# Kernel optimization log

Hardware: AMD Instinct MI355X
Metric: run time of the kernel (lower is better)

The kernel has to match this reference:

```python
import jax, jax.numpy as jnp
import numpy as np
from math import sqrt

B = 32          # batch
C = 81          # label_num (class 0 = background, skipped)
N = 15130       # number of default boxes
K = 200         # max_num candidates per class
MAX_OUT = 200   # max_output boxes per image
SCORE_THR = 0.05
CRITERIA = 0.45
SCALE_XY = 0.1
SCALE_WH = 0.2
NEG_INF = -1e30


def make_dboxes_xywh():
    """Replicates DefaultBoxes for figsize (1200,1200), SSD-R34 COCO config."""
    fig = 1200
    feat = [50, 25, 13, 7, 3, 3]
    scales = [int(s * fig / 300) for s in [21, 45, 99, 153, 207, 261, 315]]
    aspect_ratios = [[2], [2, 3], [2, 3], [2, 3], [2], [2]]
    boxes = []
    for idx, f in enumerate(feat):
        step = int(fig / f)
        fk = fig // step  # == f for this config
        sk1 = scales[idx] / fig
        sk2 = scales[idx + 1] / fig
        sk3 = sqrt(sk1 * sk2)
        sizes = [(sk1, sk1), (sk3, sk3)]
        for a in aspect_ratios[idx]:
            w, h = sk1 * sqrt(a), sk1 / sqrt(a)
            sizes.append((w, h))
            sizes.append((h, w))
        for (w, h) in sizes:
            for i in range(f):
                for j in range(f):
                    cx, cy = (j + 0.5) / fk, (i + 0.5) / fk
                    boxes.append((cx, cy, w, h))
    d = np.clip(np.array(boxes, dtype=np.float32), 0.0, 1.0)
    assert d.shape[0] == N
    return d[None, :, :]  # [1, N, 4]


def setup_inputs() -> dict:
    key = jax.random.key(0)
    k1, k2 = jax.random.split(key)
    bboxes_in = jax.random.normal(k1, (B, 4, N), dtype=jnp.float32)
    scores_in = jax.random.normal(k2, (B, C, N), dtype=jnp.float32)
    dboxes_xywh = jnp.asarray(make_dboxes_xywh())
    return {"bboxes_in": bboxes_in, "scores_in": scores_in, "dboxes_xywh": dboxes_xywh}


def scale_back_batch(bboxes_in, scores_in, dboxes_xywh):
    b = jnp.transpose(bboxes_in, (0, 2, 1))            # [B, N, 4]
    xy = SCALE_XY * b[..., :2] * dboxes_xywh[..., 2:] + dboxes_xywh[..., :2]
    wh = jnp.exp(SCALE_WH * b[..., 2:]) * dboxes_xywh[..., 2:]
    ltrb = jnp.concatenate([xy - 0.5 * wh, xy + 0.5 * wh], axis=-1)  # [B, N, 4]
    probs = jax.nn.softmax(jnp.transpose(scores_in, (0, 2, 1)), axis=-1)  # [B, N, C]
    return ltrb, probs


def pairwise_iou(b):
    """Faithful to calc_iou_tensor: the masked_fill_ on delta.clone() is a no-op
    in the original, so negative deltas are NOT clamped."""
    lt = jnp.maximum(b[:, None, :2], b[None, :, :2])
    rb = jnp.minimum(b[:, None, 2:], b[None, :, 2:])
    d = rb - lt
    inter = d[..., 0] * d[..., 1]
    area = (b[:, 2] - b[:, 0]) * (b[:, 3] - b[:, 1])
    return inter / (area[:, None] + area[None, :] - inter)  # [K, K]


def nms_one_class(boxes, score):
    """boxes [N,4], score [N] -> kept boxes [K,4], kept scores [K] (NEG_INF = dropped).
    Greedy NMS over the top-K scores in descending order, matching the original
    while-loop (ascending sort + pop-from-end)."""
    s = jnp.where(score > SCORE_THR, score, NEG_INF)
    top_s, top_i = jax.lax.top_k(s, K)         # descending
    bk = boxes[top_i]                          # [K, 4]
    iou = pairwise_iou(bk)                     # [K, K]
    rng = jnp.arange(K)
    keep0 = top_s > NEG_INF

    def body(i, keep):
        suppress = keep[i] & (iou[i] >= CRITERIA) & (rng > i)
        return keep & ~suppress

    keep = jax.lax.fori_loop(0, K, body, keep0)
    return bk, jnp.where(keep, top_s, NEG_INF)


def decode_image(boxes, probs):
    """boxes [N,4], probs [N,C] -> (boxes [MAX_OUT,4], labels [MAX_OUT], scores [MAX_OUT])."""
    cls_scores = jnp.transpose(probs[:, 1:])                    # [C-1, N] (skip background)
    bks, ss = jax.vmap(nms_one_class, in_axes=(None, 0))(boxes, cls_scores)  # [C-1,K,4],[C-1,K]
    labels = jnp.repeat(jnp.arange(1, C, dtype=jnp.int32), K)   # [(C-1)*K]
    flat_s = ss.reshape(-1)
    top_s, top_i = jax.lax.top_k(flat_s, MAX_OUT)               # global top max_output
    out_boxes = bks.reshape(-1, 4)[top_i]
    out_labels = labels[top_i]
    valid = top_s > NEG_INF
    return (jnp.where(valid[:, None], out_boxes, 0.0),
            jnp.where(valid, out_labels, 0),
            jnp.where(valid, top_s, 0.0))


def reference(bboxes_in, scores_in, dboxes_xywh):
    ltrb, probs = scale_back_batch(bboxes_in, scores_in, dboxes_xywh)
    boxes, labels, scores = jax.vmap(decode_image)(ltrb, probs)
    return boxes, labels, scores  # [B,MAX_OUT,4], [B,MAX_OUT] int32, [B,MAX_OUT]
```

## Files before the change

### kernel.cpp

```cpp
#include <hip/hip_runtime.h>
#include <cstdint>
#include <cstddef>

#define BATCH 32
#define NCLS 81
#define NFG 80
#define NBOX 15130
#define NCHUNK 60
#define TOPK 200
#define NTASK (BATCH * NFG)
#define NEG_INF -1e30f
#define GCAP 1024
#define SORTCAP 1024
#define LCAP 1920
#define SCORE_THR 0.05f
#define CRITERIA 0.45f

__global__ __launch_bounds__(256) void k1_fused(
    const float* __restrict__ bboxes,
    const float* __restrict__ scores,
    const float* __restrict__ dboxes,
    float4* __restrict__ ltrb,
    unsigned long long* __restrict__ gcand,
    int* __restrict__ gcnt)
{
    const int blk = blockIdx.x;
    const int b = blk / NCHUNK;
    const int chunk = blk - b * NCHUNK;
    const int tid = threadIdx.x;
    const int n = chunk * 256 + tid;

    __shared__ unsigned long long list[LCAP];
    __shared__ int lcnt;
    __shared__ int ccnt[NFG];
    __shared__ int cbase[NFG];

    if (tid == 0) lcnt = 0;
    if (tid < NFG) ccnt[tid] = 0;
    __syncthreads();

    float m = 0.f, s = 1.f, thrv = 1e30f;
    const float* sc = scores;

    if (n < NBOX) {
        const float* bb = bboxes + (size_t)b * 4 * NBOX + n;
        float bx = bb[0];
        float by = bb[NBOX];
        float bw = bb[2 * (size_t)NBOX];
        float bh = bb[3 * (size_t)NBOX];
        float4 d = reinterpret_cast<const float4*>(dboxes)[n];
        float xx = __fadd_rn(__fmul_rn(__fmul_rn(0.1f, bx), d.z), d.x);
        float yy = __fadd_rn(__fmul_rn(__fmul_rn(0.1f, by), d.w), d.y);
        float wx = __fmul_rn(expf(__fmul_rn(0.2f, bw)), d.z);
        float wy = __fmul_rn(expf(__fmul_rn(0.2f, bh)), d.w);
        float4 o;
        o.x = __fsub_rn(xx, __fmul_rn(0.5f, wx));
        o.y = __fsub_rn(yy, __fmul_rn(0.5f, wy));
        o.z = __fadd_rn(xx, __fmul_rn(0.5f, wx));
        o.w = __fadd_rn(yy, __fmul_rn(0.5f, wy));
        ltrb[(size_t)b * NBOX + n] = o;

        sc = scores + (size_t)b * NCLS * NBOX + n;
        {
            float vals[NCLS];
#pragma unroll
            for (int c = 0; c < NCLS; ++c) vals[c] = sc[(size_t)c * NBOX];
            m = vals[0];
#pragma unroll
            for (int c = 1; c < NCLS; ++c) m = fmaxf(m, vals[c]);
            float ss = 0.0f;
#pragma unroll
            for (int c = 0; c < NCLS; ++c) ss = __fadd_rn(ss, expf(__fsub_rn(vals[c], m)));
            s = ss;
        }
        thrv = __fsub_rn(__fadd_rn(m, logf(__fmul_rn(0.05f, s))), 1e-3f);
    }

    if (n < NBOX) {
        uintptr_t scu = (uintptr_t)sc;
        asm volatile("" : "+v"(scu));
        const float* scv = (const float*)scu;
        for (int c0 = 1; c0 < NCLS; c0 += 16) {
            float vt[16];
#pragma unroll
            for (int u = 0; u < 16; ++u) {
                int c = c0 + u;
                vt[u] = (c < NCLS) ? scv[(size_t)c * NBOX] : -1e30f;
            }
#pragma unroll
            for (int u = 0; u < 16; ++u) {
                int c = c0 + u;
                if (vt[u] > thrv) {
                    float p = __fdiv_rn(expf(__fsub_rn(vt[u], m)), s);
                    if (p > SCORE_THR) {
                        int e = atomicAdd(&lcnt, 1);
                        if (e < LCAP) {
                            list[e] = ((unsigned long long)__float_as_uint(p) << 32) |
                                      ((unsigned long long)(unsigned)(c - 1) << 24) |
                                      (unsigned long long)(unsigned)n;
                        } else {
                            int pos = atomicAdd(&gcnt[b * NFG + (c - 1)], 1);
                            if (pos < GCAP)
                                gcand[(size_t)(b * NFG + (c - 1)) * GCAP + pos] =
                                    ((unsigned long long)__float_as_uint(p) << 32) |
                                    (unsigned long long)(0xFFFFFFFFu - (unsigned)n);
                        }
                    }
                }
            }
        }
    }
    __syncthreads();

    const int E = min(lcnt, LCAP);

    for (int i = tid; i < E; i += 256) {
        int c = (int)((list[i] >> 24) & 0xFF);
        atomicAdd(&ccnt[c], 1);
    }
    __syncthreads();

    if (tid < NFG && ccnt[tid] > 0)
        cbase[tid] = atomicAdd(&gcnt[b * NFG + tid], ccnt[tid]);
    __syncthreads();
    if (tid < NFG) ccnt[tid] = 0;
    __syncthreads();

    for (int i = tid; i < E; i += 256) {
        unsigned long long e = list[i];
        int c = (int)((e >> 24) & 0xFF);
        unsigned nn = (unsigned)(e & 0xFFFFFF);
        int pos = cbase[c] + atomicAdd(&ccnt[c], 1);
        if (pos < GCAP) {
            unsigned pb = (unsigned)(e >> 32);
            gcand[(size_t)(b * NFG + c) * GCAP + pos] =
                ((unsigned long long)pb << 32) |
                (unsigned long long)(0xFFFFFFFFu - nn);
        }
    }
}

template<int NR, int J, int K>
__device__ __forceinline__ void bstep(unsigned long long (&it)[NR], const int lane) {
    if constexpr (J >= 64) {
        constexpr int M = J >> 6;
#pragma unroll
        for (int r = 0; r < NR; ++r) {
            const int rp = r ^ M;
            if (rp > r) {
                const bool desc = (((unsigned)(r << 6) & (unsigned)K) == 0u);
                unsigned long long a = it[r], bb = it[rp];
                if (desc ? (a < bb) : (a > bb)) { it[r] = bb; it[rp] = a; }
            }
        }
    } else {
#pragma unroll
        for (int r = 0; r < NR; ++r) {
            unsigned long long a = it[r];
            unsigned long long bb = __shfl_xor(a, J, 64);
            const unsigned i = ((unsigned)(r << 6)) | (unsigned)lane;
            const bool desc = ((i & (unsigned)K) == 0u);
            const bool lower = ((lane & J) == 0);
            it[r] = ((desc == lower) ? (a >= bb) : (a <= bb)) ? a : bb;
        }
    }
}

template<int NR, int K, int J>
__device__ __forceinline__ void bstage(unsigned long long (&it)[NR], const int lane) {
    bstep<NR, J, K>(it, lane);
    if constexpr (J > 1) bstage<NR, K, (J >> 1)>(it, lane);
}

template<int NR>
__device__ __forceinline__ void bsort(unsigned long long (&it)[NR], const int lane,
                                      const unsigned kmax) {
    bstage<NR, 2, 1>(it, lane);
    if (kmax >= 4)   bstage<NR, 4, 2>(it, lane);
    if (kmax >= 8)   bstage<NR, 8, 4>(it, lane);
    if (kmax >= 16)  bstage<NR, 16, 8>(it, lane);
    if (kmax >= 32)  bstage<NR, 32, 16>(it, lane);
    if (kmax >= 64)  bstage<NR, 64, 32>(it, lane);
    if constexpr (NR >= 4) {
        if (kmax >= 128) bstage<NR, 128, 64>(it, lane);
        if (kmax >= 256) bstage<NR, 256, 128>(it, lane);
    }
    if constexpr (NR >= 8)  { if (kmax >= 512)  bstage<NR, 512, 256>(it, lane); }
    if constexpr (NR >= 16) { if (kmax >= 1024) bstage<NR, 1024, 512>(it, lane); }
}

__global__ __launch_bounds__(64) void k2_nms(
    const unsigned long long* __restrict__ gcand,
    const int* __restrict__ gcnt,
    const float4* __restrict__ ltrb,
    float* __restrict__ cls_scores,
    int* __restrict__ cls_idx)
{
    const int t = blockIdx.x;
    const int b = t / NFG;
    const int lane = threadIdx.x;

    const int cl = min(gcnt[t], SORTCAP);
    const unsigned long long* gc = gcand + (size_t)t * GCAP;

    unsigned kmax = 2;
    while (kmax < (unsigned)cl) kmax <<= 1;

    unsigned long long top4[4];
    if (cl <= 256) {
        unsigned long long it[4];
#pragma unroll
        for (int r = 0; r < 4; ++r) {
            const int i = (r << 6) + lane;
            it[r] = (i < cl) ? gc[i] : 0ULL;
        }
        bsort<4>(it, lane, kmax);
#pragma unroll
        for (int r = 0; r < 4; ++r) top4[r] = it[r];
    } else if (cl <= 512) {
        unsigned long long it[8];
#pragma unroll
        for (int r = 0; r < 8; ++r) {
            const int i = (r << 6) + lane;
            it[r] = (i < cl) ? gc[i] : 0ULL;
        }
        bsort<8>(it, lane, kmax);
#pragma unroll
        for (int r = 0; r < 4; ++r) top4[r] = it[r];
    } else {
        unsigned long long it[16];
#pragma unroll
        for (int r = 0; r < 16; ++r) {
            const int i = (r << 6) + lane;
            it[r] = (i < cl) ? gc[i] : 0ULL;
        }
        bsort<16>(it, lane, kmax);
#pragma unroll
        for (int r = 0; r < 4; ++r) top4[r] = it[r];
    }

    const int mk = min(cl, TOPK);

    float4 myb[4];
    float mya[4], myp[4];
    int myn[4];
#pragma unroll
    for (int r = 0; r < 4; ++r) {
        const int i = (r << 6) + lane;
        myb[r] = make_float4(0.f, 0.f, 0.f, 0.f);
        mya[r] = 0.f; myp[r] = 0.f; myn[r] = 0;
        if (i < mk) {
            const unsigned long long key = top4[r];
            const unsigned n = 0xFFFFFFFFu - (unsigned)(key & 0xFFFFFFFFull);
            const float4 bx = ltrb[(size_t)b * NBOX + n];
            myb[r] = bx;
            mya[r] = __fmul_rn(__fsub_rn(bx.z, bx.x), __fsub_rn(bx.w, bx.y));
            myp[r] = __uint_as_float((unsigned)(key >> 32));
            myn[r] = b * NBOX + (int)n;
        }
    }

    auto maskBits = [](int r) -> unsigned long long {
        if (r <= 0) return 0ULL;
        if (r >= 64) return ~0ULL;
        return (1ULL << r) - 1ULL;
    };
    unsigned long long kw0 = maskBits(mk);
    unsigned long long kw1 = maskBits(mk - 64);
    unsigned long long kw2 = maskBits(mk - 128);
    unsigned long long kw3 = maskBits(mk - 192);

#define RDLANE_F(V, SL) __uint_as_float((unsigned)__builtin_amdgcn_readlane((int)__float_as_uint(V), (SL)))

#define NMS_QUAD(KWQ, Q)                                                           \
    {                                                                              \
        const int i0 = (Q) << 6;                                                   \
        const int i1 = min(mk, i0 + 64);                                           \
        for (int i = i0; i < i1; ++i) {                                            \
            if ((KWQ >> (i - i0)) & 1ULL) {                                        \
                const int sl = i - i0;                                             \
                const float bix = RDLANE_F(myb[Q].x, sl);                          \
                const float biy = RDLANE_F(myb[Q].y, sl);                          \
                const float biz = RDLANE_F(myb[Q].z, sl);                          \
                const float biw = RDLANE_F(myb[Q].w, sl);                          \
                const float ai  = RDLANE_F(mya[Q], sl);                            \
                _Pragma("unroll")                                                  \
                for (int q2 = 0; q2 < 4; ++q2) {                                   \
                    const int j = (q2 << 6) + lane;                                \
                    const float4 bj = myb[q2];                                     \
                    const float ltx = fmaxf(bix, bj.x), lty = fmaxf(biy, bj.y);    \
                    const float rbx = fminf(biz, bj.z), rby = fminf(biw, bj.w);    \
                    const float dx = __fsub_rn(rbx, ltx), dy = __fsub_rn(rby, lty);\
                    const float inter = __fmul_rn(dx, dy);                         \
                    const float uni = __fsub_rn(__fadd_rn(ai, mya[q2]), inter);    \
                    const float iou = __fdiv_rn(inter, uni);                       \
                    const unsigned long long sup =                                 \
                        __ballot((iou >= CRITERIA) && (j > i));                    \
                    if (q2 == 0) kw0 &= ~sup;                                      \
                    else if (q2 == 1) kw1 &= ~sup;                                 \
                    else if (q2 == 2) kw2 &= ~sup;                                 \
                    else kw3 &= ~sup;                                              \
                }                                                                  \
            }                                                                      \
        }                                                                          \
    }
    NMS_QUAD(kw0, 0)
    NMS_QUAD(kw1, 1)
    NMS_QUAD(kw2, 2)
    NMS_QUAD(kw3, 3)
#undef NMS_QUAD
#undef RDLANE_F

#pragma unroll
    for (int r = 0; r < 4; ++r) {
        const int i = (r << 6) + lane;
        if (i < TOPK) {
            const unsigned long long kq = (r == 0) ? kw0 : (r == 1) ? kw1
                                         : (r == 2) ? kw2 : kw3;
            const bool keep = (i < mk) && ((kq >> lane) & 1ULL);
            cls_scores[(size_t)t * TOPK + i] = keep ? myp[r] : NEG_INF;
            if (i < mk) cls_idx[(size_t)t * TOPK + i] = myn[r];
        }
    }
}

__device__ __forceinline__ int blockReduceSum(int x, int* red, int tid) {
    __syncthreads();
    red[tid] = x;
    __syncthreads();
    for (int off = 128; off > 0; off >>= 1) {
        if (tid < off) red[tid] += red[tid + off];
        __syncthreads();
    }
    return red[0];
}

__global__ __launch_bounds__(256) void k3_topk(
    const float* __restrict__ cls_scores,
    const int* __restrict__ cls_idx,
    const float4* __restrict__ ltrb,
    float* __restrict__ out)
{
    const int b = blockIdx.x;
    const int tid = threadIdx.x;
    const int NFLAT = NFG * TOPK;
    const int PER = 63;

    __shared__ unsigned long long sel[512];
    __shared__ int scnt;
    __shared__ int red[256];

    const float* S = cls_scores + (size_t)b * NFLAT;
    float v[PER];
#pragma unroll
    for (int i = 0; i < PER; ++i) {
        int j = i * 256 + tid;
        v[i] = (j < NFLAT) ? S[j] : NEG_INF;
    }

    int lc = 0;
#pragma unroll
    for (int i = 0; i < PER; ++i) lc += (v[i] > -1e29f) ? 1 : 0;
    int validCount = blockReduceSum(lc, red, tid);

    unsigned thrBits = 0;
    if (validCount > TOPK) {
        unsigned lo = 0, hi = 0x7F800000u;
        while (lo < hi) {
            unsigned mid = (lo + hi) >> 1;
            float mf = __uint_as_float(mid);
            int c2 = 0;
#pragma unroll
            for (int i = 0; i < PER; ++i) c2 += (v[i] > mf) ? 1 : 0;
            int tot = blockReduceSum(c2, red, tid);
            if (tot < TOPK) hi = mid; else lo = mid + 1;
        }
        thrBits = lo;
    }

    __syncthreads();
    if (tid == 0) scnt = 0;
    for (int i = tid; i < 512; i += 256) sel[i] = 0ULL;
    __syncthreads();

    const bool useGE = (validCount > TOPK);
    const float thrF = __uint_as_float(thrBits);
#pragma unroll
    for (int i = 0; i < PER; ++i) {
        int j = i * 256 + tid;
        bool take = useGE ? (v[i] >= thrF) : (v[i] > -1e29f);
        if (j < NFLAT && take) {
            int pos = atomicAdd(&scnt, 1);
            if (pos < 512) {
                sel[pos] = ((unsigned long long)__float_as_uint(v[i]) << 32) |
                           (unsigned long long)(0xFFFFFFFFu - (unsigned)j);
            }
        }
    }
    __syncthreads();
    int total = min(min(scnt, 512), TOPK);

    for (unsigned k = 2; k <= 512; k <<= 1) {
        for (unsigned j = k >> 1; j > 0; j >>= 1) {
            for (unsigned i = tid; i < 512; i += 256) {
                unsigned ixj = i ^ j;
                if (ixj > i) {
                    unsigned long long a = sel[i], bb2 = sel[ixj];
                    bool desc = ((i & k) == 0);
                    if (desc ? (a < bb2) : (a > bb2)) { sel[i] = bb2; sel[ixj] = a; }
                }
            }
            __syncthreads();
        }
    }

    if (tid < TOPK) {
        size_t ob = (size_t)b * TOPK + tid;
        float4 bx = make_float4(0.f, 0.f, 0.f, 0.f);
        float lab = 0.f, sc2 = 0.f;
        if (tid < total) {
            unsigned long long key = sel[tid];
            unsigned j = 0xFFFFFFFFu - (unsigned)(key & 0xFFFFFFFFull);
            sc2 = __uint_as_float((unsigned)(key >> 32));
            unsigned cls = j / TOPK;
            int gi = cls_idx[(size_t)b * NFLAT + j];
            bx = ltrb[gi];
            lab = (float)(cls + 1);
        }
        reinterpret_cast<float4*>(out)[ob] = bx;
        out[(size_t)BATCH * TOPK * 4 + ob] = lab;
        out[(size_t)BATCH * TOPK * 4 + (size_t)BATCH * TOPK + ob] = sc2;
    }
}

extern "C" void kernel_launch(void* const* d_in, const int* in_sizes, int n_in,
                              void* d_out, int out_size, void* d_ws, size_t ws_size,
                              hipStream_t stream) {
    (void)in_sizes; (void)n_in; (void)out_size; (void)ws_size;
    const float* bboxes = (const float*)d_in[0];
    const float* scores = (const float*)d_in[1];
    const float* dboxes = (const float*)d_in[2];
    float* out = (float*)d_out;

    char* ws = (char*)d_ws;
    size_t off = 0;
    float4* ltrb = (float4*)(ws + off);      off += (size_t)BATCH * NBOX * 16;
    unsigned long long* gcand = (unsigned long long*)(ws + off);
                                             off += (size_t)NTASK * GCAP * 8;
    float* cls_scores = (float*)(ws + off);  off += (size_t)NTASK * TOPK * 4;
    int*   cls_idx    = (int*)(ws + off);    off += (size_t)NTASK * TOPK * 4;
    int*   gcnt       = (int*)(ws + off);    off += (size_t)NTASK * 4;

    hipMemsetAsync(gcnt, 0, NTASK * sizeof(int), stream);

    k1_fused<<<BATCH * NCHUNK, 256, 0, stream>>>(bboxes, scores, dboxes, ltrb, gcand, gcnt);
    k2_nms<<<NTASK, 64, 0, stream>>>(gcand, gcnt, ltrb, cls_scores, cls_idx);
    k3_topk<<<BATCH, 256, 0, stream>>>(cls_scores, cls_idx, ltrb, out);
}
```

Before: 205.2 us.

## Precompute next NMS suppression row speculatively, use wave-level reductions and register sort in topk

The NMS loop now computes the suppression ballots for row i+1 before deciding whether row i is kept, so the IoU math no longer waits on the keep-bit dependency, and it skips column blocks that lie before the current one. This removes the serial dependence and branch from the critical path, at the cost of computing rows that turn out to be suppressed. The top-k kernel replaces its shared-memory tree reduction with wavefront shuffle reductions and replaces the 256-thread shared-memory bitonic sort, which needed a barrier per stage, with a single-wave register bitonic sort.

```diff
diff --git a/kernel.cpp b/kernel.cpp
--- a/kernel.cpp
+++ b/kernel.cpp
@@ -189,6 +189,56 @@
     if constexpr (NR >= 16) { if (kmax >= 1024) bstage<NR, 1024, 512>(it, lane); }
 }
 
+__device__ __forceinline__ float rdlaneF(float v, int sl) {
+    return __uint_as_float((unsigned)__builtin_amdgcn_readlane((int)__float_as_uint(v), sl));
+}
+
+template<int Q>
+__device__ __forceinline__ void supRow(const float4 (&myb)[4], const float (&mya)[4],
+                                       int i, int lane, unsigned long long (&S)[4]) {
+    const int sl = i & 63;
+    const float bix = rdlaneF(myb[Q].x, sl);
+    const float biy = rdlaneF(myb[Q].y, sl);
+    const float biz = rdlaneF(myb[Q].z, sl);
+    const float biw = rdlaneF(myb[Q].w, sl);
+    const float ai  = rdlaneF(mya[Q], sl);
+#pragma unroll
+    for (int q2 = 0; q2 < 4; ++q2) {
+        if (q2 < Q) { S[q2] = 0ULL; continue; }
+        const int j = (q2 << 6) + lane;
+        const float4 bj = myb[q2];
+        const float ltx = fmaxf(bix, bj.x), lty = fmaxf(biy, bj.y);
+        const float rbx = fminf(biz, bj.z), rby = fminf(biw, bj.w);
+        const float dx = __fsub_rn(rbx, ltx), dy = __fsub_rn(rby, lty);
+        const float inter = __fmul_rn(dx, dy);
+        const float uni = __fsub_rn(__fadd_rn(ai, mya[q2]), inter);
+        const float iou = __fdiv_rn(inter, uni);
+        const bool after = (q2 > Q) ? true : (j > i);
+        S[q2] = __ballot((iou >= CRITERIA) && after);
+    }
+}
+
+template<int Q>
+__device__ __forceinline__ void nmsQuad(const float4 (&myb)[4], const float (&mya)[4],
+                                        unsigned long long (&kw)[4], int mk, int lane) {
+    const int i0 = Q << 6;
+    const int i1 = min(mk, i0 + 64);
+    if (i0 >= i1) return;
+    unsigned long long Sc[4], Sn[4];
+    supRow<Q>(myb, mya, i0, lane, Sc);
+    for (int i = i0; i < i1; ++i) {
+        const int inx = (i + 1 < i1) ? (i + 1) : i;
+        supRow<Q>(myb, mya, inx, lane, Sn);
+        if ((kw[Q] >> (i - i0)) & 1ULL) {
+#pragma unroll
+            for (int q2 = 0; q2 < 4; ++q2)
+                if (q2 >= Q) kw[q2] &= ~Sc[q2];
+        }
+#pragma unroll
+        for (int q2 = 0; q2 < 4; ++q2) Sc[q2] = Sn[q2];
+    }
+}
+
 __global__ __launch_bounds__(64) void k2_nms(
     const unsigned long long* __restrict__ gcand,
     const int* __restrict__ gcnt,
@@ -265,74 +315,35 @@
         if (r >= 64) return ~0ULL;
         return (1ULL << r) - 1ULL;
     };
-    unsigned long long kw0 = maskBits(mk);
-    unsigned long long kw1 = maskBits(mk - 64);
-    unsigned long long kw2 = maskBits(mk - 128);
-    unsigned long long kw3 = maskBits(mk - 192);
-
-#define RDLANE_F(V, SL) __uint_as_float((unsigned)__builtin_amdgcn_readlane((int)__float_as_uint(V), (SL)))
-
-#define NMS_QUAD(KWQ, Q)                                                           \
-    {                                                                              \
-        const int i0 = (Q) << 6;                                                   \
-        const int i1 = min(mk, i0 + 64);                                           \
-        for (int i = i0; i < i1; ++i) {                                            \
-            if ((KWQ >> (i - i0)) & 1ULL) {                                        \
-                const int sl = i - i0;                                             \
-                const float bix = RDLANE_F(myb[Q].x, sl);                          \
-                const float biy = RDLANE_F(myb[Q].y, sl);                          \
-                const float biz = RDLANE_F(myb[Q].z, sl);                          \
-                const float biw = RDLANE_F(myb[Q].w, sl);                          \
-                const float ai  = RDLANE_F(mya[Q], sl);                            \
-                _Pragma("unroll")                                                  \
-                for (int q2 = 0; q2 < 4; ++q2) {                                   \
-                    const int j = (q2 << 6) + lane;                                \
-                    const float4 bj = myb[q2];                                     \
-                    const float ltx = fmaxf(bix, bj.x), lty = fmaxf(biy, bj.y);    \
-                    const float rbx = fminf(biz, bj.z), rby = fminf(biw, bj.w);    \
-                    const float dx = __fsub_rn(rbx, ltx), dy = __fsub_rn(rby, lty);\
-                    const float inter = __fmul_rn(dx, dy);                         \
-                    const float uni = __fsub_rn(__fadd_rn(ai, mya[q2]), inter);    \
-                    const float iou = __fdiv_rn(inter, uni);                       \
-                    const unsigned long long sup =                                 \
-                        __ballot((iou >= CRITERIA) && (j > i));                    \
-                    if (q2 == 0) kw0 &= ~sup;                                      \
-                    else if (q2 == 1) kw1 &= ~sup;                                 \
-                    else if (q2 == 2) kw2 &= ~sup;                                 \
-                    else kw3 &= ~sup;                                              \
-                }                                                                  \
-            }                                                                      \
-        }                                                                          \
-    }
-    NMS_QUAD(kw0, 0)
-    NMS_QUAD(kw1, 1)
-    NMS_QUAD(kw2, 2)
-    NMS_QUAD(kw3, 3)
-#undef NMS_QUAD
-#undef RDLANE_F
+    unsigned long long kw[4];
+    kw[0] = maskBits(mk);
+    kw[1] = maskBits(mk - 64);
+    kw[2] = maskBits(mk - 128);
+    kw[3] = maskBits(mk - 192);
+
+    nmsQuad<0>(myb, mya, kw, mk, lane);
+    nmsQuad<1>(myb, mya, kw, mk, lane);
+    nmsQuad<2>(myb, mya, kw, mk, lane);
+    nmsQuad<3>(myb, mya, kw, mk, lane);
 
 #pragma unroll
     for (int r = 0; r < 4; ++r) {
         const int i = (r << 6) + lane;
         if (i < TOPK) {
-            const unsigned long long kq = (r == 0) ? kw0 : (r == 1) ? kw1
-                                         : (r == 2) ? kw2 : kw3;
-            const bool keep = (i < mk) && ((kq >> lane) & 1ULL);
+            const bool keep = (i < mk) && ((kw[r] >> lane) & 1ULL);
             cls_scores[(size_t)t * TOPK + i] = keep ? myp[r] : NEG_INF;
             if (i < mk) cls_idx[(size_t)t * TOPK + i] = myn[r];
         }
     }
 }
 
-__device__ __forceinline__ int blockReduceSum(int x, int* red, int tid) {
-    __syncthreads();
-    red[tid] = x;
-    __syncthreads();
-    for (int off = 128; off > 0; off >>= 1) {
-        if (tid < off) red[tid] += red[tid + off];
-        __syncthreads();
-    }
-    return red[0];
+__device__ __forceinline__ int blockSum4(int x, int* red4, int tid) {
+#pragma unroll
+    for (int s = 1; s < 64; s <<= 1) x += __shfl_xor(x, s, 64);
+    __syncthreads();
+    if ((tid & 63) == 0) red4[tid >> 6] = x;
+    __syncthreads();
+    return red4[0] + red4[1] + red4[2] + red4[3];
 }
 
 __global__ __launch_bounds__(256) void k3_topk(
@@ -348,7 +359,7 @@
 
     __shared__ unsigned long long sel[512];
     __shared__ int scnt;
-    __shared__ int red[256];
+    __shared__ int red4[4];
 
     const float* S = cls_scores + (size_t)b * NFLAT;
     float v[PER];
@@ -361,7 +372,7 @@
     int lc = 0;
 #pragma unroll
     for (int i = 0; i < PER; ++i) lc += (v[i] > -1e29f) ? 1 : 0;
-    int validCount = blockReduceSum(lc, red, tid);
+    int validCount = blockSum4(lc, red4, tid);
 
     unsigned thrBits = 0;
     if (validCount > TOPK) {
@@ -372,7 +383,7 @@
             int c2 = 0;
 #pragma unroll
             for (int i = 0; i < PER; ++i) c2 += (v[i] > mf) ? 1 : 0;
-            int tot = blockReduceSum(c2, red, tid);
+            int tot = blockSum4(c2, red4, tid);
             if (tot < TOPK) hi = mid; else lo = mid + 1;
         }
         thrBits = lo;
@@ -400,19 +411,15 @@
     __syncthreads();
     int total = min(min(scnt, 512), TOPK);
 
-    for (unsigned k = 2; k <= 512; k <<= 1) {
-        for (unsigned j = k >> 1; j > 0; j >>= 1) {
-            for (unsigned i = tid; i < 512; i += 256) {
-                unsigned ixj = i ^ j;
-                if (ixj > i) {
-                    unsigned long long a = sel[i], bb2 = sel[ixj];
-                    bool desc = ((i & k) == 0);
-                    if (desc ? (a < bb2) : (a > bb2)) { sel[i] = bb2; sel[ixj] = a; }
-                }
-            }
-            __syncthreads();
-        }
-    }
+    if (tid < 64) {
+        unsigned long long it[8];
+#pragma unroll
+        for (int r = 0; r < 8; ++r) it[r] = sel[(r << 6) + tid];
+        bsort<8>(it, tid, 512);
+#pragma unroll
+        for (int r = 0; r < 8; ++r) sel[(r << 6) + tid] = it[r];
+    }
+    __syncthreads();
 
     if (tid < TOPK) {
         size_t ob = (size_t)b * TOPK + tid;
```

New measurement: 270.0 us. 1.32x slower.

## Skip lower-triangle NMS blocks, use wave-shuffle reductions and single-wave register sort

Applied to the files above, without the earlier changes.

In the NMS loop, a box in quad Q no longer tests against boxes in earlier quads, since those can never be suppressed by a later box. In the top-k kernel, the shared-memory tree reduction is replaced by wave shuffles plus a 4-entry cross-wave sum, cutting the barriers per binary-search step. The block-wide shared-memory bitonic sort is replaced by a register bitonic sort in one wavefront, using an existing bsort helper. This trades the many block barriers for work done by a single wave while the other waves sit idle.

```diff
diff --git a/kernel.cpp b/kernel.cpp
--- a/kernel.cpp
+++ b/kernel.cpp
@@ -286,6 +286,7 @@
                 const float ai  = RDLANE_F(mya[Q], sl);                            \
                 _Pragma("unroll")                                                  \
                 for (int q2 = 0; q2 < 4; ++q2) {                                   \
+                    if (q2 < (Q)) continue;      \
                     const int j = (q2 << 6) + lane;                                \
                     const float4 bj = myb[q2];                                     \
                     const float ltx = fmaxf(bix, bj.x), lty = fmaxf(biy, bj.y);    \
@@ -324,15 +325,13 @@
     }
 }
 
-__device__ __forceinline__ int blockReduceSum(int x, int* red, int tid) {
-    __syncthreads();
-    red[tid] = x;
-    __syncthreads();
-    for (int off = 128; off > 0; off >>= 1) {
-        if (tid < off) red[tid] += red[tid + off];
-        __syncthreads();
-    }
-    return red[0];
+__device__ __forceinline__ int blockSum4(int x, int* red4, int tid) {
+#pragma unroll
+    for (int s = 1; s < 64; s <<= 1) x += __shfl_xor(x, s, 64);
+    __syncthreads();
+    if ((tid & 63) == 0) red4[tid >> 6] = x;
+    __syncthreads();
+    return red4[0] + red4[1] + red4[2] + red4[3];
 }
 
 __global__ __launch_bounds__(256) void k3_topk(
@@ -348,7 +347,7 @@
 
     __shared__ unsigned long long sel[512];
     __shared__ int scnt;
-    __shared__ int red[256];
+    __shared__ int red4[4];
 
     const float* S = cls_scores + (size_t)b * NFLAT;
     float v[PER];
@@ -361,7 +360,7 @@
     int lc = 0;
 #pragma unroll
     for (int i = 0; i < PER; ++i) lc += (v[i] > -1e29f) ? 1 : 0;
-    int validCount = blockReduceSum(lc, red, tid);
+    int validCount = blockSum4(lc, red4, tid);
 
     unsigned thrBits = 0;
     if (validCount > TOPK) {
@@ -372,7 +371,7 @@
             int c2 = 0;
 #pragma unroll
             for (int i = 0; i < PER; ++i) c2 += (v[i] > mf) ? 1 : 0;
-            int tot = blockReduceSum(c2, red, tid);
+            int tot = blockSum4(c2, red4, tid);
             if (tot < TOPK) hi = mid; else lo = mid + 1;
         }
         thrBits = lo;
@@ -400,19 +399,15 @@
     __syncthreads();
     int total = min(min(scnt, 512), TOPK);
 
-    for (unsigned k = 2; k <= 512; k <<= 1) {
-        for (unsigned j = k >> 1; j > 0; j >>= 1) {
-            for (unsigned i = tid; i < 512; i += 256) {
-                unsigned ixj = i ^ j;
-                if (ixj > i) {
-                    unsigned long long a = sel[i], bb2 = sel[ixj];
-                    bool desc = ((i & k) == 0);
-                    if (desc ? (a < bb2) : (a > bb2)) { sel[i] = bb2; sel[ixj] = a; }
-                }
-            }
-            __syncthreads();
-        }
-    }
+    if (tid < 64) {
+        unsigned long long it[8];
+#pragma unroll
+        for (int r = 0; r < 8; ++r) it[r] = sel[(r << 6) + tid];
+        bsort<8>(it, tid, 512);
+#pragma unroll
+        for (int r = 0; r < 8; ++r) sel[(r << 6) + tid] = it[r];
+    }
+    __syncthreads();
 
     if (tid < TOPK) {
         size_t ob = (size_t)b * TOPK + tid;
```

Result: no change. 205.8 us (median of 2 runs) (+0.3%).
